# Optimization experiments

Hardware: AMD Instinct MI355X
Metric: run time of the kernel (lower is better)

The kernel has to match this reference:

```python
import jax, jax.numpy as jnp
import numpy as np

B, NC, F, V, D = 16384, 13, 26, 100000, 16
H1, H2 = 400, 400
DNN_IN = NC + F * D  # 13 + 416 = 429


def setup_inputs() -> dict:
    key = jax.random.key(0)
    ks = jax.random.split(key, 12)
    s = 0.02
    return {
        "continuous": jax.random.normal(ks[0], (B, NC), jnp.float32),
        "cat_idx": jax.random.randint(ks[1], (B, F), 0, V),
        "W_cont": jax.random.normal(ks[2], (NC, 1), jnp.float32) * s,
        "b_cont": jnp.zeros((1,), jnp.float32),
        "emb_first": jax.random.normal(ks[3], (F, V), jnp.float32) * s,
        "emb": jax.random.normal(ks[4], (F, V, D), jnp.float32) * s,
        "W1": jax.random.normal(ks[5], (DNN_IN, H1), jnp.float32) * s,
        "b1": jnp.zeros((H1,), jnp.float32),
        "W2": jax.random.normal(ks[6], (H1, H2), jnp.float32) * s,
        "b2": jnp.zeros((H2,), jnp.float32),
        "W_out": jax.random.normal(ks[7], (H2 + 1, 1), jnp.float32) * s,
        "b_out": jnp.zeros((1,), jnp.float32),
    }


def reference(continuous, cat_idx, W_cont, b_cont, emb_first, emb, W1, b1, W2, b2, W_out, b_out):
    f_ids = jnp.arange(F)  # column ids
    # FM first-order: continuous linear + per-column 1-dim embedding gather, summed over columns
    fm1_cat = emb_first[f_ids[None, :], cat_idx]          # [B, F]
    fm1 = continuous @ W_cont + b_cont + jnp.sum(fm1_cat, axis=1, keepdims=True)  # [B, 1]
    # FM second-order: per-column D-dim embedding gather
    E = emb[f_ids[None, :], cat_idx]                      # [B, F, D]
    sum_emb = jnp.sum(E, axis=1)                          # [B, D]
    fm2 = 0.5 * jnp.sum(sum_emb * sum_emb - jnp.sum(E * E, axis=1), axis=1, keepdims=True)  # [B, 1]
    fm_out = fm1 + fm2
    # DNN on [continuous | flattened embeddings]; Dropout(0.0) is identity
    dnn_in = jnp.concatenate([continuous, E.reshape(E.shape[0], -1)], axis=1)  # [B, 429]
    h = jax.nn.relu(dnn_in @ W1 + b1)
    h = jax.nn.relu(h @ W2 + b2)
    fusion = jnp.concatenate([fm_out, h], axis=1)         # [B, H2+1]
    return fusion @ W_out + b_out                          # [B, 1]
```

## Files before the change

### kernel.cpp

```cpp
#include <hip/hip_runtime.h>
#include <hip/hip_bf16.h>
#include <stdint.h>

#define NB    16384
#define NCONT 13
#define NF    26
#define NV    100000
#define ND    16
#define NH    400
#define K1    448
#define K2    416
#define NPAD  512

typedef __attribute__((ext_vector_type(8))) __bf16 bf16x8;
typedef __attribute__((ext_vector_type(8))) short short8;
typedef __attribute__((ext_vector_type(4))) float f32x4;

__device__ __forceinline__ short f2bf(float x) {
  union { float f; uint32_t u; } c; c.f = x;
  uint32_t r = (c.u + 0x7FFFu + ((c.u >> 16) & 1u)) >> 16;
  return (short)(uint16_t)r;
}

__device__ __forceinline__ void load16(const void* g, void* l) {
  __builtin_amdgcn_global_load_lds(
      (const __attribute__((address_space(1))) void*)g,
      (__attribute__((address_space(3))) void*)l, 16, 0, 0);
}

__global__ __launch_bounds__(256)
void prep_k(const float* __restrict__ W1, const float* __restrict__ W2,
            short* __restrict__ W1T, short* __restrict__ W2T) {
  int t = blockIdx.x * 256 + threadIdx.x;
  if (t < NPAD * K1) {
    int n = t / K1, k = t - n * K1;
    float v = 0.f;
    if (n < NH) {
      if (k < 416)       v = W1[(size_t)(13 + k) * NH + n];
      else if (k < 429)  v = W1[(size_t)(k - 416) * NH + n];
    }
    W1T[t] = f2bf(v);
  } else {
    int u = t - NPAD * K1;
    int n = u / K2, k = u - n * K2;
    float v = (n < NH && k < NH) ? W2[(size_t)k * NH + n] : 0.f;
    W2T[u] = f2bf(v);
  }
}

__global__ __launch_bounds__(256)
void gather_k(const float* __restrict__ cont, const int* __restrict__ cat,
              const float* __restrict__ Wc, const float* __restrict__ bc,
              const float* __restrict__ emb1, const float* __restrict__ emb,
              const float* __restrict__ Wout, const float* __restrict__ bout,
              short* __restrict__ dnn, float* __restrict__ out) {
  int t = blockIdx.x * 256 + threadIdx.x;
  int b = t >> 2;
  int q = t & 3;
  int f0 = (26 * q) >> 2;
  int f1 = (26 * (q + 1)) >> 2;
  float se[16];
#pragma unroll
  for (int d = 0; d < 16; d++) se[d] = 0.f;
  float sumsq = 0.f, fm1 = 0.f;
  short* drow = dnn + (size_t)b * K1;

  for (int f = f0; f < f1; f++) {
    int idx = cat[b * NF + f];
    const float4* ep = (const float4*)(emb + ((size_t)f * NV + idx) * ND);
    float4 e0 = ep[0], e1 = ep[1], e2 = ep[2], e3 = ep[3];
    fm1 += emb1[(size_t)f * NV + idx];
    se[0] += e0.x; se[1] += e0.y; se[2] += e0.z; se[3] += e0.w;
    se[4] += e1.x; se[5] += e1.y; se[6] += e1.z; se[7] += e1.w;
    se[8] += e2.x; se[9] += e2.y; se[10] += e2.z; se[11] += e2.w;
    se[12] += e3.x; se[13] += e3.y; se[14] += e3.z; se[15] += e3.w;
    sumsq += e0.x*e0.x + e0.y*e0.y + e0.z*e0.z + e0.w*e0.w
           + e1.x*e1.x + e1.y*e1.y + e1.z*e1.z + e1.w*e1.w
           + e2.x*e2.x + e2.y*e2.y + e2.z*e2.z + e2.w*e2.w
           + e3.x*e3.x + e3.y*e3.y + e3.z*e3.z + e3.w*e3.w;
    short8 p0, p1;
    p0[0]=f2bf(e0.x); p0[1]=f2bf(e0.y); p0[2]=f2bf(e0.z); p0[3]=f2bf(e0.w);
    p0[4]=f2bf(e1.x); p0[5]=f2bf(e1.y); p0[6]=f2bf(e1.z); p0[7]=f2bf(e1.w);
    p1[0]=f2bf(e2.x); p1[1]=f2bf(e2.y); p1[2]=f2bf(e2.z); p1[3]=f2bf(e2.w);
    p1[4]=f2bf(e3.x); p1[5]=f2bf(e3.y); p1[6]=f2bf(e3.z); p1[7]=f2bf(e3.w);
    *(short8*)(drow + f * 16) = p0;
    *(short8*)(drow + f * 16 + 8) = p1;
  }
#pragma unroll
  for (int d = 0; d < 16; d++) {
    se[d] += __shfl_xor(se[d], 1, 64);
    se[d] += __shfl_xor(se[d], 2, 64);
  }
  sumsq += __shfl_xor(sumsq, 1, 64);
  sumsq += __shfl_xor(sumsq, 2, 64);
  fm1   += __shfl_xor(fm1, 1, 64);
  fm1   += __shfl_xor(fm1, 2, 64);

  if (q == 0) {
    float s2 = 0.f;
#pragma unroll
    for (int d = 0; d < 16; d++) s2 += se[d] * se[d];
    float fm2 = 0.5f * (s2 - sumsq);
    float fmc = bc[0];
    short tail[32];
#pragma unroll
    for (int i = 0; i < 13; i++) {
      float c = cont[(size_t)b * NCONT + i];
      fmc += c * Wc[i];
      tail[i] = f2bf(c);
    }
#pragma unroll
    for (int i = 13; i < 32; i++) tail[i] = 0;
#pragma unroll
    for (int v2 = 0; v2 < 4; v2++) {
      short8 tv;
#pragma unroll
      for (int e = 0; e < 8; e++) tv[e] = tail[v2 * 8 + e];
      *(short8*)(drow + 416 + v2 * 8) = tv;
    }
    out[b] = (fm1 + fmc + fm2) * Wout[0] + bout[0];
  }
}

template <int K>
__device__ __forceinline__ void gemm_core(const short* __restrict__ A,
                                          const short* __restrict__ Bt,
                                          short* lA, short* lB,
                                          int bm, int bn, int tid,
                                          f32x4 acc[4][4]) {
  const int lane = tid & 63;
  const int wave = tid >> 6;
  const int wm = (wave & 1) * 64;
  const int wn = (wave >> 1) * 64;
  const int lrow = lane & 15;
  const int quad = lane >> 4;
  const int r0 = tid >> 2, s0 = (tid & 3) * 8;
  const short* gA0 = A + (size_t)(bm + r0) * K + s0;
  const short* gA1 = A + (size_t)(bm + r0 + 64) * K + s0;
  const short* gB0 = Bt + (size_t)(bn + r0) * K + s0;
  const short* gB1 = Bt + (size_t)(bn + r0 + 64) * K + s0;
  short* lA0 = lA + tid * 8;
  short* lA1 = lA + (tid + 256) * 8;
  short* lB0 = lB + tid * 8;
  short* lB1 = lB + (tid + 256) * 8;

  for (int k0 = 0; k0 < K; k0 += 32) {
    __syncthreads();
    load16(gA0 + k0, lA0);
    load16(gA1 + k0, lA1);
    load16(gB0 + k0, lB0);
    load16(gB1 + k0, lB1);
    __syncthreads();
    bf16x8 af[4], bfr[4];
#pragma unroll
    for (int i = 0; i < 4; i++)
      af[i] = *(const bf16x8*)(lA + (wm + i * 16 + lrow) * 32 + quad * 8);
#pragma unroll
    for (int j = 0; j < 4; j++)
      bfr[j] = *(const bf16x8*)(lB + (wn + j * 16 + lrow) * 32 + quad * 8);
#pragma unroll
    for (int i = 0; i < 4; i++)
#pragma unroll
      for (int j = 0; j < 4; j++)
        acc[i][j] = __builtin_amdgcn_mfma_f32_16x16x32_bf16(af[i], bfr[j], acc[i][j], 0, 0, 0);
  }
}

__global__ __launch_bounds__(256, 2)
void gemm1_k(const short* __restrict__ A, const short* __restrict__ Bt,
             const float* __restrict__ b1, short* __restrict__ H) {
  __shared__ short lA[128 * 32];
  __shared__ short lB[128 * 32];
  f32x4 acc[4][4];
#pragma unroll
  for (int i = 0; i < 4; i++)
#pragma unroll
    for (int j = 0; j < 4; j++)
#pragma unroll
      for (int r = 0; r < 4; r++) acc[i][j][r] = 0.f;
  int tid = threadIdx.x;
  int bm = blockIdx.y * 128, bn = blockIdx.x * 128;
  gemm_core<K1>(A, Bt, lA, lB, bm, bn, tid, acc);

  int lane = tid & 63, wave = tid >> 6;
  int wm = (wave & 1) * 64, wn = (wave >> 1) * 64;
  int lrow = lane & 15, quad = lane >> 4;
#pragma unroll
  for (int j = 0; j < 4; j++) {
    int col = bn + wn + j * 16 + lrow;
    if (col >= K2) continue;
    bool pad = (col >= NH);
    float bias = pad ? 0.f : b1[col];
#pragma unroll
    for (int i = 0; i < 4; i++) {
#pragma unroll
      for (int r = 0; r < 4; r++) {
        int row = bm + wm + i * 16 + quad * 4 + r;
        float v = pad ? 0.f : fmaxf(acc[i][j][r] + bias, 0.f);
        H[(size_t)row * K2 + col] = f2bf(v);
      }
    }
  }
}

__global__ __launch_bounds__(256, 2)
void gemm2_k(const short* __restrict__ A, const short* __restrict__ Bt,
             const float* __restrict__ b2, const float* __restrict__ Wout,
             float* __restrict__ out) {
  __shared__ short lA[128 * 32];
  __shared__ short lB[128 * 32];
  f32x4 acc[4][4];
#pragma unroll
  for (int i = 0; i < 4; i++)
#pragma unroll
    for (int j = 0; j < 4; j++)
#pragma unroll
      for (int r = 0; r < 4; r++) acc[i][j][r] = 0.f;
  int tid = threadIdx.x;
  int bm = blockIdx.y * 128, bn = blockIdx.x * 128;
  gemm_core<K2>(A, Bt, lA, lB, bm, bn, tid, acc);

  int lane = tid & 63, wave = tid >> 6;
  int wm = (wave & 1) * 64, wn = (wave >> 1) * 64;
  int lrow = lane & 15, quad = lane >> 4;
  float bw[4], wo[4];
#pragma unroll
  for (int j = 0; j < 4; j++) {
    int col = bn + wn + j * 16 + lrow;
    bw[j] = (col < NH) ? b2[col] : 0.f;
    wo[j] = (col < NH) ? Wout[1 + col] : 0.f;
  }
#pragma unroll
  for (int i = 0; i < 4; i++) {
#pragma unroll
    for (int r = 0; r < 4; r++) {
      float s = 0.f;
#pragma unroll
      for (int j = 0; j < 4; j++)
        s += fmaxf(acc[i][j][r] + bw[j], 0.f) * wo[j];
      s += __shfl_xor(s, 1, 64);
      s += __shfl_xor(s, 2, 64);
      s += __shfl_xor(s, 4, 64);
      s += __shfl_xor(s, 8, 64);
      if (lrow == 0) {
        int row = bm + wm + i * 16 + quad * 4 + r;
        atomicAdd(&out[row], s);
      }
    }
  }
}

extern "C" void kernel_launch(void* const* d_in, const int* in_sizes, int n_in,
                              void* d_out, int out_size, void* d_ws, size_t ws_size,
                              hipStream_t stream) {
  const float* cont   = (const float*)d_in[0];
  const int*   cat    = (const int*)d_in[1];
  const float* W_cont = (const float*)d_in[2];
  const float* b_cont = (const float*)d_in[3];
  const float* emb1   = (const float*)d_in[4];
  const float* emb    = (const float*)d_in[5];
  const float* W1     = (const float*)d_in[6];
  const float* b1     = (const float*)d_in[7];
  const float* W2     = (const float*)d_in[8];
  const float* b2     = (const float*)d_in[9];
  const float* W_out  = (const float*)d_in[10];
  const float* b_out  = (const float*)d_in[11];
  float* out = (float*)d_out;

  char* ws = (char*)d_ws;
  size_t off = 0;
  short* dnn = (short*)(ws + off); off += (size_t)NB * K1 * 2;
  short* W1T = (short*)(ws + off); off += (size_t)NPAD * K1 * 2;
  short* W2T = (short*)(ws + off); off += (size_t)NPAD * K2 * 2;
  short* H   = (short*)(ws + off); off += (size_t)NB * K2 * 2;
  (void)ws_size; (void)in_sizes; (void)n_in; (void)out_size;

  prep_k<<<dim3((NPAD * K1 + NPAD * K2) / 256), dim3(256), 0, stream>>>(W1, W2, W1T, W2T);
  gather_k<<<dim3(NB * 4 / 256), dim3(256), 0, stream>>>(cont, cat, W_cont, b_cont,
                                                         emb1, emb, W_out, b_out, dnn, out);
  gemm1_k<<<dim3(4, NB / 128), dim3(256), 0, stream>>>(dnn, W1T, b1, H);
  gemm2_k<<<dim3(4, NB / 128), dim3(256), 0, stream>>>(H, W2T, b2, W_out, out);
}
```

Before: 287.1 us.

## Fuse embedding gather and both MLP GEMMs into one per-row-tile kernel

Replaces the separate gather, GEMM1 and GEMM2 kernels with one kernel. Each 256-thread block handles 32 batch rows: it gathers the embeddings into padded LDS, runs layer 1 with MFMA into an LDS hidden tile, then runs layer 2 and reduces into the output with atomics. This removes the global round-trips of the dnn input and hidden activations, plus two launches. In exchange, every block streams the full transposed weight matrices from global/L2 with register double-buffering instead of sharing LDS tiles, and each block has fewer rows over which to amortize that weight traffic and hide gather latency.

Result: faster. 281.4 us (-2.0%).

```diff
diff --git a/kernel.cpp b/kernel.cpp
--- a/kernel.cpp
+++ b/kernel.cpp
@@ -9,8 +9,11 @@
 #define ND    16
 #define NH    400
 #define K1    448
+#define KP1   456
 #define K2    416
+#define KP2   424
 #define NPAD  512
+#define ROWS  32
 
 typedef __attribute__((ext_vector_type(8))) __bf16 bf16x8;
 typedef __attribute__((ext_vector_type(8))) short short8;
@@ -20,12 +23,6 @@
   union { float f; uint32_t u; } c; c.f = x;
   uint32_t r = (c.u + 0x7FFFu + ((c.u >> 16) & 1u)) >> 16;
   return (short)(uint16_t)r;
-}
-
-__device__ __forceinline__ void load16(const void* g, void* l) {
-  __builtin_amdgcn_global_load_lds(
-      (const __attribute__((address_space(1))) void*)g,
-      (__attribute__((address_space(3))) void*)l, 16, 0, 0);
 }
 
 __global__ __launch_bounds__(256)
@@ -48,203 +45,203 @@
   }
 }
 
-__global__ __launch_bounds__(256)
-void gather_k(const float* __restrict__ cont, const int* __restrict__ cat,
-              const float* __restrict__ Wc, const float* __restrict__ bc,
-              const float* __restrict__ emb1, const float* __restrict__ emb,
-              const float* __restrict__ Wout, const float* __restrict__ bout,
-              short* __restrict__ dnn, float* __restrict__ out) {
-  int t = blockIdx.x * 256 + threadIdx.x;
-  int b = t >> 2;
-  int q = t & 3;
-  int f0 = (26 * q) >> 2;
-  int f1 = (26 * (q + 1)) >> 2;
-  float se[16];
-#pragma unroll
-  for (int d = 0; d < 16; d++) se[d] = 0.f;
-  float sumsq = 0.f, fm1 = 0.f;
-  short* drow = dnn + (size_t)b * K1;
-
-  for (int f = f0; f < f1; f++) {
-    int idx = cat[b * NF + f];
-    const float4* ep = (const float4*)(emb + ((size_t)f * NV + idx) * ND);
-    float4 e0 = ep[0], e1 = ep[1], e2 = ep[2], e3 = ep[3];
-    fm1 += emb1[(size_t)f * NV + idx];
-    se[0] += e0.x; se[1] += e0.y; se[2] += e0.z; se[3] += e0.w;
-    se[4] += e1.x; se[5] += e1.y; se[6] += e1.z; se[7] += e1.w;
-    se[8] += e2.x; se[9] += e2.y; se[10] += e2.z; se[11] += e2.w;
-    se[12] += e3.x; se[13] += e3.y; se[14] += e3.z; se[15] += e3.w;
-    sumsq += e0.x*e0.x + e0.y*e0.y + e0.z*e0.z + e0.w*e0.w
-           + e1.x*e1.x + e1.y*e1.y + e1.z*e1.z + e1.w*e1.w
-           + e2.x*e2.x + e2.y*e2.y + e2.z*e2.z + e2.w*e2.w
-           + e3.x*e3.x + e3.y*e3.y + e3.z*e3.z + e3.w*e3.w;
-    short8 p0, p1;
-    p0[0]=f2bf(e0.x); p0[1]=f2bf(e0.y); p0[2]=f2bf(e0.z); p0[3]=f2bf(e0.w);
-    p0[4]=f2bf(e1.x); p0[5]=f2bf(e1.y); p0[6]=f2bf(e1.z); p0[7]=f2bf(e1.w);
-    p1[0]=f2bf(e2.x); p1[1]=f2bf(e2.y); p1[2]=f2bf(e2.z); p1[3]=f2bf(e2.w);
-    p1[4]=f2bf(e3.x); p1[5]=f2bf(e3.y); p1[6]=f2bf(e3.z); p1[7]=f2bf(e3.w);
-    *(short8*)(drow + f * 16) = p0;
-    *(short8*)(drow + f * 16 + 8) = p1;
-  }
-#pragma unroll
-  for (int d = 0; d < 16; d++) {
-    se[d] += __shfl_xor(se[d], 1, 64);
-    se[d] += __shfl_xor(se[d], 2, 64);
-  }
-  sumsq += __shfl_xor(sumsq, 1, 64);
-  sumsq += __shfl_xor(sumsq, 2, 64);
-  fm1   += __shfl_xor(fm1, 1, 64);
-  fm1   += __shfl_xor(fm1, 2, 64);
-
-  if (q == 0) {
-    float s2 = 0.f;
-#pragma unroll
-    for (int d = 0; d < 16; d++) s2 += se[d] * se[d];
-    float fm2 = 0.5f * (s2 - sumsq);
-    float fmc = bc[0];
-    short tail[32];
-#pragma unroll
-    for (int i = 0; i < 13; i++) {
-      float c = cont[(size_t)b * NCONT + i];
-      fmc += c * Wc[i];
-      tail[i] = f2bf(c);
-    }
-#pragma unroll
-    for (int i = 13; i < 32; i++) tail[i] = 0;
-#pragma unroll
-    for (int v2 = 0; v2 < 4; v2++) {
-      short8 tv;
-#pragma unroll
-      for (int e = 0; e < 8; e++) tv[e] = tail[v2 * 8 + e];
-      *(short8*)(drow + 416 + v2 * 8) = tv;
-    }
-    out[b] = (fm1 + fmc + fm2) * Wout[0] + bout[0];
-  }
-}
-
-template <int K>
-__device__ __forceinline__ void gemm_core(const short* __restrict__ A,
-                                          const short* __restrict__ Bt,
-                                          short* lA, short* lB,
-                                          int bm, int bn, int tid,
-                                          f32x4 acc[4][4]) {
+__global__ __launch_bounds__(256, 2)
+void fused_k(const float* __restrict__ cont, const int* __restrict__ cat,
+             const float* __restrict__ Wc, const float* __restrict__ bc,
+             const float* __restrict__ emb1, const float* __restrict__ emb,
+             const short* __restrict__ W1T, const float* __restrict__ b1,
+             const short* __restrict__ W2T, const float* __restrict__ b2,
+             const float* __restrict__ Wout, const float* __restrict__ bout,
+             float* __restrict__ out) {
+  __shared__ short lA[ROWS * KP1];
+  __shared__ short lH[ROWS * KP2];
+  const int tid = threadIdx.x;
+  const int bm = blockIdx.x * ROWS;
+
+  {
+    const int q  = tid & 7;
+    const int rl = tid >> 3;
+    const int b  = bm + rl;
+    const int f0 = (NF * q) >> 3;
+    const int f1 = (NF * (q + 1)) >> 3;
+    float se[16];
+#pragma unroll
+    for (int d = 0; d < 16; d++) se[d] = 0.f;
+    float sumsq = 0.f, fm1 = 0.f;
+
+    for (int f = f0; f < f1; f++) {
+      int idx = cat[(size_t)b * NF + f];
+      const float4* ep = (const float4*)(emb + ((size_t)f * NV + idx) * ND);
+      float4 e0 = ep[0], e1 = ep[1], e2 = ep[2], e3 = ep[3];
+      fm1 += emb1[(size_t)f * NV + idx];
+      se[0] += e0.x; se[1] += e0.y; se[2] += e0.z; se[3] += e0.w;
+      se[4] += e1.x; se[5] += e1.y; se[6] += e1.z; se[7] += e1.w;
+      se[8] += e2.x; se[9] += e2.y; se[10] += e2.z; se[11] += e2.w;
+      se[12] += e3.x; se[13] += e3.y; se[14] += e3.z; se[15] += e3.w;
+      sumsq += e0.x*e0.x + e0.y*e0.y + e0.z*e0.z + e0.w*e0.w
+             + e1.x*e1.x + e1.y*e1.y + e1.z*e1.z + e1.w*e1.w
+             + e2.x*e2.x + e2.y*e2.y + e2.z*e2.z + e2.w*e2.w
+             + e3.x*e3.x + e3.y*e3.y + e3.z*e3.z + e3.w*e3.w;
+      short8 p0, p1;
+      p0[0]=f2bf(e0.x); p0[1]=f2bf(e0.y); p0[2]=f2bf(e0.z); p0[3]=f2bf(e0.w);
+      p0[4]=f2bf(e1.x); p0[5]=f2bf(e1.y); p0[6]=f2bf(e1.z); p0[7]=f2bf(e1.w);
+      p1[0]=f2bf(e2.x); p1[1]=f2bf(e2.y); p1[2]=f2bf(e2.z); p1[3]=f2bf(e2.w);
+      p1[4]=f2bf(e3.x); p1[5]=f2bf(e3.y); p1[6]=f2bf(e3.z); p1[7]=f2bf(e3.w);
+      *(short8*)&lA[rl * KP1 + f * 16]     = p0;
+      *(short8*)&lA[rl * KP1 + f * 16 + 8] = p1;
+    }
+#pragma unroll
+    for (int d = 0; d < 16; d++) {
+      se[d] += __shfl_xor(se[d], 1, 64);
+      se[d] += __shfl_xor(se[d], 2, 64);
+      se[d] += __shfl_xor(se[d], 4, 64);
+    }
+    sumsq += __shfl_xor(sumsq, 1, 64);
+    sumsq += __shfl_xor(sumsq, 2, 64);
+    sumsq += __shfl_xor(sumsq, 4, 64);
+    fm1   += __shfl_xor(fm1, 1, 64);
+    fm1   += __shfl_xor(fm1, 2, 64);
+    fm1   += __shfl_xor(fm1, 4, 64);
+
+    if (q == 0) {
+      float s2 = 0.f;
+#pragma unroll
+      for (int d = 0; d < 16; d++) s2 += se[d] * se[d];
+      float fm2 = 0.5f * (s2 - sumsq);
+      float fmc = bc[0];
+      short tail[32];
+#pragma unroll
+      for (int i = 0; i < NCONT; i++) {
+        float c = cont[(size_t)b * NCONT + i];
+        fmc += c * Wc[i];
+        tail[i] = f2bf(c);
+      }
+#pragma unroll
+      for (int i = NCONT; i < 32; i++) tail[i] = 0;
+#pragma unroll
+      for (int v = 0; v < 4; v++) {
+        short8 tv;
+#pragma unroll
+        for (int e = 0; e < 8; e++) tv[e] = tail[v * 8 + e];
+        *(short8*)&lA[rl * KP1 + 416 + v * 8] = tv;
+      }
+      out[b] = (fm1 + fmc + fm2) * Wout[0] + bout[0];
+    }
+  }
+  __syncthreads();
+
   const int lane = tid & 63;
   const int wave = tid >> 6;
-  const int wm = (wave & 1) * 64;
-  const int wn = (wave >> 1) * 64;
   const int lrow = lane & 15;
   const int quad = lane >> 4;
-  const int r0 = tid >> 2, s0 = (tid & 3) * 8;
-  const short* gA0 = A + (size_t)(bm + r0) * K + s0;
-  const short* gA1 = A + (size_t)(bm + r0 + 64) * K + s0;
-  const short* gB0 = Bt + (size_t)(bn + r0) * K + s0;
-  const short* gB1 = Bt + (size_t)(bn + r0 + 64) * K + s0;
-  short* lA0 = lA + tid * 8;
-  short* lA1 = lA + (tid + 256) * 8;
-  short* lB0 = lB + tid * 8;
-  short* lB1 = lB + (tid + 256) * 8;
-
-  for (int k0 = 0; k0 < K; k0 += 32) {
-    __syncthreads();
-    load16(gA0 + k0, lA0);
-    load16(gA1 + k0, lA1);
-    load16(gB0 + k0, lB0);
-    load16(gB1 + k0, lB1);
-    __syncthreads();
-    bf16x8 af[4], bfr[4];
-#pragma unroll
-    for (int i = 0; i < 4; i++)
-      af[i] = *(const bf16x8*)(lA + (wm + i * 16 + lrow) * 32 + quad * 8);
-#pragma unroll
-    for (int j = 0; j < 4; j++)
-      bfr[j] = *(const bf16x8*)(lB + (wn + j * 16 + lrow) * 32 + quad * 8);
-#pragma unroll
-    for (int i = 0; i < 4; i++)
-#pragma unroll
-      for (int j = 0; j < 4; j++)
-        acc[i][j] = __builtin_amdgcn_mfma_f32_16x16x32_bf16(af[i], bfr[j], acc[i][j], 0, 0, 0);
-  }
-}
-
-__global__ __launch_bounds__(256, 2)
-void gemm1_k(const short* __restrict__ A, const short* __restrict__ Bt,
-             const float* __restrict__ b1, short* __restrict__ H) {
-  __shared__ short lA[128 * 32];
-  __shared__ short lB[128 * 32];
-  f32x4 acc[4][4];
-#pragma unroll
-  for (int i = 0; i < 4; i++)
-#pragma unroll
-    for (int j = 0; j < 4; j++)
+  const int wn   = wave * 128;
+  const int kq   = quad * 8;
+  f32x4 acc[2][8];
+
+#pragma unroll
+  for (int i = 0; i < 2; i++)
+#pragma unroll
+    for (int j = 0; j < 8; j++)
 #pragma unroll
       for (int r = 0; r < 4; r++) acc[i][j][r] = 0.f;
-  int tid = threadIdx.x;
-  int bm = blockIdx.y * 128, bn = blockIdx.x * 128;
-  gemm_core<K1>(A, Bt, lA, lB, bm, bn, tid, acc);
-
-  int lane = tid & 63, wave = tid >> 6;
-  int wm = (wave & 1) * 64, wn = (wave >> 1) * 64;
-  int lrow = lane & 15, quad = lane >> 4;
-#pragma unroll
-  for (int j = 0; j < 4; j++) {
-    int col = bn + wn + j * 16 + lrow;
-    if (col >= K2) continue;
-    bool pad = (col >= NH);
-    float bias = pad ? 0.f : b1[col];
-#pragma unroll
-    for (int i = 0; i < 4; i++) {
+  {
+    const short* wp[8];
+#pragma unroll
+    for (int j = 0; j < 8; j++)
+      wp[j] = W1T + (size_t)(wn + j * 16 + lrow) * K1 + kq;
+    bf16x8 wf[2][8], af[2][2];
+#pragma unroll
+    for (int j = 0; j < 8; j++) wf[0][j] = *(const bf16x8*)(wp[j]);
+#pragma unroll
+    for (int i = 0; i < 2; i++) af[0][i] = *(const bf16x8*)&lA[(i * 16 + lrow) * KP1 + kq];
+#pragma unroll
+    for (int ks = 0; ks < K1 / 32; ks++) {
+      const int cur = ks & 1, nxt = cur ^ 1;
+      if (ks + 1 < K1 / 32) {
+#pragma unroll
+        for (int j = 0; j < 8; j++) wf[nxt][j] = *(const bf16x8*)(wp[j] + (ks + 1) * 32);
+#pragma unroll
+        for (int i = 0; i < 2; i++)
+          af[nxt][i] = *(const bf16x8*)&lA[(i * 16 + lrow) * KP1 + (ks + 1) * 32 + kq];
+      }
+#pragma unroll
+      for (int i = 0; i < 2; i++)
+#pragma unroll
+        for (int j = 0; j < 8; j++)
+          acc[i][j] = __builtin_amdgcn_mfma_f32_16x16x32_bf16(af[cur][i], wf[cur][j], acc[i][j], 0, 0, 0);
+    }
+  }
+#pragma unroll
+  for (int j = 0; j < 8; j++) {
+    int col = wn + j * 16 + lrow;
+    if (col < K2) {
+      float bias = (col < NH) ? b1[col] : 0.f;
+#pragma unroll
+      for (int i = 0; i < 2; i++)
+#pragma unroll
+        for (int r = 0; r < 4; r++) {
+          int row = i * 16 + quad * 4 + r;
+          float v = (col < NH) ? fmaxf(acc[i][j][r] + bias, 0.f) : 0.f;
+          lH[row * KP2 + col] = f2bf(v);
+        }
+    }
+  }
+  __syncthreads();
+
+#pragma unroll
+  for (int i = 0; i < 2; i++)
+#pragma unroll
+    for (int j = 0; j < 8; j++)
+#pragma unroll
+      for (int r = 0; r < 4; r++) acc[i][j][r] = 0.f;
+  {
+    const short* wp[8];
+#pragma unroll
+    for (int j = 0; j < 8; j++)
+      wp[j] = W2T + (size_t)(wn + j * 16 + lrow) * K2 + kq;
+    bf16x8 wf[2][8], af[2][2];
+#pragma unroll
+    for (int j = 0; j < 8; j++) wf[0][j] = *(const bf16x8*)(wp[j]);
+#pragma unroll
+    for (int i = 0; i < 2; i++) af[0][i] = *(const bf16x8*)&lH[(i * 16 + lrow) * KP2 + kq];
+#pragma unroll
+    for (int ks = 0; ks < K2 / 32; ks++) {
+      const int cur = ks & 1, nxt = cur ^ 1;
+      if (ks + 1 < K2 / 32) {
+#pragma unroll
+        for (int j = 0; j < 8; j++) wf[nxt][j] = *(const bf16x8*)(wp[j] + (ks + 1) * 32);
+#pragma unroll
+        for (int i = 0; i < 2; i++)
+          af[nxt][i] = *(const bf16x8*)&lH[(i * 16 + lrow) * KP2 + (ks + 1) * 32 + kq];
+      }
+#pragma unroll
+      for (int i = 0; i < 2; i++)
+#pragma unroll
+        for (int j = 0; j < 8; j++)
+          acc[i][j] = __builtin_amdgcn_mfma_f32_16x16x32_bf16(af[cur][i], wf[cur][j], acc[i][j], 0, 0, 0);
+    }
+  }
+  {
+    float bw[8], wo[8];
+#pragma unroll
+    for (int j = 0; j < 8; j++) {
+      int col = wn + j * 16 + lrow;
+      bw[j] = (col < NH) ? b2[col] : 0.f;
+      wo[j] = (col < NH) ? Wout[1 + col] : 0.f;
+    }
+#pragma unroll
+    for (int i = 0; i < 2; i++) {
 #pragma unroll
       for (int r = 0; r < 4; r++) {
-        int row = bm + wm + i * 16 + quad * 4 + r;
-        float v = pad ? 0.f : fmaxf(acc[i][j][r] + bias, 0.f);
-        H[(size_t)row * K2 + col] = f2bf(v);
-      }
-    }
-  }
-}
-
-__global__ __launch_bounds__(256, 2)
-void gemm2_k(const short* __restrict__ A, const short* __restrict__ Bt,
-             const float* __restrict__ b2, const float* __restrict__ Wout,
-             float* __restrict__ out) {
-  __shared__ short lA[128 * 32];
-  __shared__ short lB[128 * 32];
-  f32x4 acc[4][4];
-#pragma unroll
-  for (int i = 0; i < 4; i++)
-#pragma unroll
-    for (int j = 0; j < 4; j++)
-#pragma unroll
-      for (int r = 0; r < 4; r++) acc[i][j][r] = 0.f;
-  int tid = threadIdx.x;
-  int bm = blockIdx.y * 128, bn = blockIdx.x * 128;
-  gemm_core<K2>(A, Bt, lA, lB, bm, bn, tid, acc);
-
-  int lane = tid & 63, wave = tid >> 6;
-  int wm = (wave & 1) * 64, wn = (wave >> 1) * 64;
-  int lrow = lane & 15, quad = lane >> 4;
-  float bw[4], wo[4];
-#pragma unroll
-  for (int j = 0; j < 4; j++) {
-    int col = bn + wn + j * 16 + lrow;
-    bw[j] = (col < NH) ? b2[col] : 0.f;
-    wo[j] = (col < NH) ? Wout[1 + col] : 0.f;
-  }
-#pragma unroll
-  for (int i = 0; i < 4; i++) {
-#pragma unroll
-    for (int r = 0; r < 4; r++) {
-      float s = 0.f;
-#pragma unroll
-      for (int j = 0; j < 4; j++)
-        s += fmaxf(acc[i][j][r] + bw[j], 0.f) * wo[j];
-      s += __shfl_xor(s, 1, 64);
-      s += __shfl_xor(s, 2, 64);
-      s += __shfl_xor(s, 4, 64);
-      s += __shfl_xor(s, 8, 64);
-      if (lrow == 0) {
-        int row = bm + wm + i * 16 + quad * 4 + r;
-        atomicAdd(&out[row], s);
+        float s = 0.f;
+#pragma unroll
+        for (int j = 0; j < 8; j++)
+          s += fmaxf(acc[i][j][r] + bw[j], 0.f) * wo[j];
+        s += __shfl_xor(s, 1, 64);
+        s += __shfl_xor(s, 2, 64);
+        s += __shfl_xor(s, 4, 64);
+        s += __shfl_xor(s, 8, 64);
+        if (lrow == 0) atomicAdd(&out[bm + i * 16 + quad * 4 + r], s);
       }
     }
   }
@@ -268,16 +265,12 @@
   float* out = (float*)d_out;
 
   char* ws = (char*)d_ws;
-  size_t off = 0;
-  short* dnn = (short*)(ws + off); off += (size_t)NB * K1 * 2;
-  short* W1T = (short*)(ws + off); off += (size_t)NPAD * K1 * 2;
-  short* W2T = (short*)(ws + off); off += (size_t)NPAD * K2 * 2;
-  short* H   = (short*)(ws + off); off += (size_t)NB * K2 * 2;
+  short* W1T = (short*)ws;
+  short* W2T = (short*)(ws + (size_t)NPAD * K1 * 2);
   (void)ws_size; (void)in_sizes; (void)n_in; (void)out_size;
 
   prep_k<<<dim3((NPAD * K1 + NPAD * K2) / 256), dim3(256), 0, stream>>>(W1, W2, W1T, W2T);
-  gather_k<<<dim3(NB * 4 / 256), dim3(256), 0, stream>>>(cont, cat, W_cont, b_cont,
-                                                         emb1, emb, W_out, b_out, dnn, out);
-  gemm1_k<<<dim3(4, NB / 128), dim3(256), 0, stream>>>(dnn, W1T, b1, H);
-  gemm2_k<<<dim3(4, NB / 128), dim3(256), 0, stream>>>(H, W2T, b2, W_out, out);
-}
+  fused_k<<<dim3(NB / ROWS), dim3(256), 0, stream>>>(cont, cat, W_cont, b_cont,
+                                                     emb1, emb, W1T, b1, W2T, b2,
+                                                     W_out, b_out, out);
+}
```
